# Kernel optimization log

Measured on AMD Instinct MI355X. Metric: run time of the kernel, lower is better.

The kernel has to match this reference:

```python
import jax, jax.numpy as jnp
import numpy as np

CHUNK = 64


def setup_inputs() -> dict:
    key = jax.random.key(0)
    ks = jax.random.split(key, 5)
    B, H, S, K, V = 2, 8, 8192, 128, 128
    q = jax.random.normal(ks[0], (B, H, S, K), jnp.float32)
    k = jax.random.normal(ks[1], (B, H, S, K), jnp.float32)
    v = jax.random.normal(ks[2], (B, H, S, V), jnp.float32)
    # decay gate is a (typically negative) log-decay
    g = -0.1 * jax.random.uniform(ks[3], (B, H, S), jnp.float32)
    beta = jax.random.uniform(ks[4], (B, H, S), jnp.float32)
    return {"q": q, "k": k, "v": v, "g": g, "beta": beta}


def _gated_delta_chunkwise(q, k, v, g, beta, chunk_size=CHUNK):
    B, H, S, K = q.shape
    V = v.shape[-1]
    scale = K ** -0.5
    # L2-normalize q/k, scale q
    q = q / (jnp.linalg.norm(q, axis=-1, keepdims=True) + 1e-6)
    k = k / (jnp.linalg.norm(k, axis=-1, keepdims=True) + 1e-6)
    q = (q * scale).astype(jnp.float32)
    k = k.astype(jnp.float32)
    v = v.astype(jnp.float32)
    g = g.astype(jnp.float32)
    beta = beta.astype(jnp.float32)

    BT = chunk_size
    assert S % BT == 0, "seq_len must be a multiple of chunk_size in this reference"
    N = S // BT
    # reshape into chunks: [N, B, H, BT, ...]
    qc = jnp.transpose(q.reshape(B, H, N, BT, K), (2, 0, 1, 3, 4))
    kc = jnp.transpose(k.reshape(B, H, N, BT, K), (2, 0, 1, 3, 4))
    vc = jnp.transpose(v.reshape(B, H, N, BT, V), (2, 0, 1, 3, 4))
    gc = jnp.transpose(g.reshape(B, H, N, BT), (2, 0, 1, 3))
    bc = jnp.transpose(beta.reshape(B, H, N, BT), (2, 0, 1, 3))

    gc = jnp.cumsum(gc, axis=-1)            # within-chunk cumulative log-decay
    eg = jnp.exp(gc)                        # [N,B,H,BT]

    # pairwise relative decay within chunk: d[i,j] = g_i - g_j  (<=0 for j<=i when g is non-increasing)
    d = gc[..., :, None] - gc[..., None, :]          # [N,B,H,BT,BT]
    de = jnp.minimum(d, 0.0)
    strict = jnp.tril(jnp.ones((BT, BT), bool), -1)
    incl = jnp.tril(jnp.ones((BT, BT), bool), 0)
    exp_s = jnp.exp(jnp.where(strict, de, -jnp.inf))  # strictly lower
    exp_i = jnp.exp(jnp.where(incl, de, -jnp.inf))    # inclusive lower

    # M = I + beta_i * (k_i . k_j) * exp(g_i - g_j), strictly lower triangular
    A0 = jnp.einsum('nbhik,nbhjk->nbhij', kc, kc) * exp_s * bc[..., :, None]
    M = jnp.eye(BT, dtype=jnp.float32) + A0
    Aqk = jnp.einsum('nbhik,nbhjk->nbhij', qc, kc) * exp_i

    # WY solve: M [w|u] = [beta*k*exp(g) | beta*v]
    rhs = jnp.concatenate([bc[..., None] * kc * eg[..., None], bc[..., None] * vc], axis=-1)
    solved = jax.lax.linalg.triangular_solve(M, rhs, left_side=True, lower=True, unit_diagonal=True)
    w = solved[..., :K]
    u = solved[..., K:]

    S0 = jnp.zeros((B, H, K, V), jnp.float32)

    def step(St, inp):
        q_i, k_i, u_i, g_i, w_i, A_i, eg_i = inp
        v_i = u_i - jnp.einsum('bhck,bhkv->bhcv', w_i, St)
        o_inter = jnp.einsum('bhck,bhkv->bhcv', q_i * eg_i[..., None], St)
        o_intra = jnp.einsum('bhij,bhjv->bhiv', A_i, v_i)
        o = o_inter + o_intra
        eg_last = eg_i[:, :, -1]
        ratio = jnp.where(eg_i > 0.0, eg_last[:, :, None] / eg_i, 0.0)
        S_new = St * eg_last[..., None, None] + jnp.einsum('bhck,bhcv->bhkv', ratio[..., None] * k_i, v_i)
        return S_new, o

    Sf, oc = jax.lax.scan(step, S0, (qc, kc, u, gc, w, Aqk, eg))
    o = jnp.transpose(oc, (1, 2, 0, 3, 4)).reshape(B, H, S, V)
    return o, Sf


def reference(q, k, v, g, beta):
    return _gated_delta_chunkwise(q, k, v, g, beta)
```

## Files before the change

### kernel.cpp

```cpp
#include <hip/hip_runtime.h>
#include <hip/hip_bf16.h>

typedef __bf16 bf16_t;
typedef bf16_t bf16x8 __attribute__((ext_vector_type(8)));
typedef float  f32x4  __attribute__((ext_vector_type(4)));

#define MFMA16(a, b, c) __builtin_amdgcn_mfma_f32_16x16x32_bf16((a), (b), (c), 0, 0, 0)

static constexpr int BH_N  = 16;
static constexpr int S_LEN = 8192;
static constexpr int KD    = 128;
static constexpr int VD    = 128;
static constexpr int BT    = 64;
static constexpr int NCH   = S_LEN / BT;
static constexpr int NT    = BH_N * NCH;

static constexpr size_t WS_W_OFF   = 0;
static constexpr size_t WS_Q_OFF   = WS_W_OFF   + (size_t)NT*BT*KD*2;
static constexpr size_t WS_KRT_OFF = WS_Q_OFF   + (size_t)NT*BT*KD*2;
static constexpr size_t WS_AQK_OFF = WS_KRT_OFF + (size_t)NT*KD*BT*2;
static constexpr size_t WS_U_OFF   = WS_AQK_OFF + (size_t)NT*BT*BT*2;
static constexpr size_t WS_EGL_OFF = WS_U_OFF   + (size_t)NT*BT*KD*4;

__global__ __launch_bounds__(256) void gdn_pre(
    const float* __restrict__ qg, const float* __restrict__ kg, const float* __restrict__ vg,
    const float* __restrict__ gg, const float* __restrict__ bg,
    bf16_t* __restrict__ wsW, bf16_t* __restrict__ wsQ, bf16_t* __restrict__ wsKrT,
    bf16_t* __restrict__ wsAqk, float* __restrict__ wsU, float* __restrict__ wsEgl)
{
    __shared__ bf16_t sKb[64][136];
    __shared__ bf16_t sQb[64][136];
    __shared__ float  sA0[64][64];
    __shared__ float  sGc[64];
    __shared__ float  sEg[64];
    __shared__ float  sBeta[64];

    const int tid  = threadIdx.x;
    const int lane = tid & 63;
    const int wid  = tid >> 6;
    const int tile = blockIdx.x;
    const int bh   = tile >> 7;
    const int c    = tile & 127;
    const size_t rowbase = (size_t)bh * S_LEN + (size_t)c * BT;

    if (wid == 0) {
        float val = gg[rowbase + lane];
        #pragma unroll
        for (int off = 1; off < 64; off <<= 1) {
            float t = __shfl_up(val, off);
            if (lane >= off) val += t;
        }
        sGc[lane] = val;
        sEg[lane] = expf(val);
    } else if (wid == 1) {
        sBeta[lane] = bg[rowbase + lane];
    }

    {
        const int r = tid >> 2;
        const int p = tid & 3;
        const float4* kp = reinterpret_cast<const float4*>(kg + (rowbase + r) * KD + p * 32);
        float4 kv[8];
        float ss = 0.f;
        #pragma unroll
        for (int ii = 0; ii < 8; ++ii) {
            kv[ii] = kp[ii];
            ss += kv[ii].x*kv[ii].x + kv[ii].y*kv[ii].y + kv[ii].z*kv[ii].z + kv[ii].w*kv[ii].w;
        }
        ss += __shfl_xor(ss, 1);
        ss += __shfl_xor(ss, 2);
        float inv = 1.f / (sqrtf(ss) + 1e-6f);
        #pragma unroll
        for (int ii = 0; ii < 8; ++ii) {
            int cb = p * 32 + ii * 4;
            sKb[r][cb+0] = (bf16_t)(kv[ii].x * inv);
            sKb[r][cb+1] = (bf16_t)(kv[ii].y * inv);
            sKb[r][cb+2] = (bf16_t)(kv[ii].z * inv);
            sKb[r][cb+3] = (bf16_t)(kv[ii].w * inv);
        }
        const float4* qp = reinterpret_cast<const float4*>(qg + (rowbase + r) * KD + p * 32);
        float4 qv[8];
        ss = 0.f;
        #pragma unroll
        for (int ii = 0; ii < 8; ++ii) {
            qv[ii] = qp[ii];
            ss += qv[ii].x*qv[ii].x + qv[ii].y*qv[ii].y + qv[ii].z*qv[ii].z + qv[ii].w*qv[ii].w;
        }
        ss += __shfl_xor(ss, 1);
        ss += __shfl_xor(ss, 2);
        inv = 0.08838834764831845f / (sqrtf(ss) + 1e-6f);
        #pragma unroll
        for (int ii = 0; ii < 8; ++ii) {
            int cb = p * 32 + ii * 4;
            sQb[r][cb+0] = (bf16_t)(qv[ii].x * inv);
            sQb[r][cb+1] = (bf16_t)(qv[ii].y * inv);
            sQb[r][cb+2] = (bf16_t)(qv[ii].z * inv);
            sQb[r][cb+3] = (bf16_t)(qv[ii].w * inv);
        }
    }
    __syncthreads();

    {
        const int frow = lane & 15;
        const int kgrp = (lane >> 4) * 8;
        f32x4 accK[4], accQ[4];
        #pragma unroll
        for (int n = 0; n < 4; ++n) { accK[n] = (f32x4){0.f,0.f,0.f,0.f}; accQ[n] = (f32x4){0.f,0.f,0.f,0.f}; }
        #pragma unroll
        for (int kk = 0; kk < 4; ++kk) {
            bf16x8 aK = *(const bf16x8*)&sKb[wid*16 + frow][kk*32 + kgrp];
            bf16x8 aQ = *(const bf16x8*)&sQb[wid*16 + frow][kk*32 + kgrp];
            #pragma unroll
            for (int n = 0; n < 4; ++n) {
                bf16x8 b = *(const bf16x8*)&sKb[n*16 + frow][kk*32 + kgrp];
                accK[n] = MFMA16(aK, b, accK[n]);
                accQ[n] = MFMA16(aQ, b, accQ[n]);
            }
        }
        const int crow = wid*16 + (lane >> 4) * 4;
        bf16_t* aqkBase = wsAqk + (size_t)tile * BT * BT;
        #pragma unroll
        for (int n = 0; n < 4; ++n) {
            #pragma unroll
            for (int r4 = 0; r4 < 4; ++r4) {
                int i = crow + r4, j = n*16 + frow;
                float e = expf(fminf(sGc[i] - sGc[j], 0.f));
                sA0[i][j] = (j < i) ? accK[n][r4] * e * sBeta[i] : 0.f;
                float aq  = (j <= i) ? accQ[n][r4] * e : 0.f;
                aqkBase[i * BT + j] = (bf16_t)aq;
            }
        }
    }

    {
        bf16_t* qb = wsQ   + (size_t)tile * BT * KD;
        bf16_t* kb = wsKrT + (size_t)tile * KD * BT;
        #pragma unroll
        for (int it = 0; it < 32; ++it) {
            int idx = tid + it * 256;
            int i = idx >> 7, m = idx & 127;
            qb[idx] = (bf16_t)((float)sQb[i][m] * sEg[i]);
        }
        #pragma unroll
        for (int it = 0; it < 32; ++it) {
            int idx = tid + it * 256;
            int m = idx >> 6, i = idx & 63;
            float ratio = expf(sGc[63] - sGc[i]);
            kb[idx] = (bf16_t)((float)sKb[i][m] * ratio);
        }
        if (tid == 0) wsEgl[tile] = sEg[63];
    }
    __syncthreads();

    {
        float x[64];
        if (tid < 128) {
            #pragma unroll
            for (int i = 0; i < 64; ++i)
                x[i] = sBeta[i] * sEg[i] * (float)sKb[i][tid];
        } else {
            const float* vp = vg + rowbase * VD + (tid - 128);
            #pragma unroll
            for (int i = 0; i < 64; ++i)
                x[i] = sBeta[i] * vp[(size_t)i * VD];
        }
        #pragma unroll
        for (int i = 1; i < 64; ++i) {
            float acc = x[i];
            #pragma unroll
            for (int j = 0; j < i; ++j)
                acc = fmaf(-sA0[i][j], x[j], acc);
            x[i] = acc;
        }
        if (tid < 128) {
            bf16_t* wp = wsW + (size_t)tile * BT * KD + tid;
            #pragma unroll
            for (int i = 0; i < 64; ++i) wp[(size_t)i * KD] = (bf16_t)x[i];
        } else {
            float* up = wsU + (size_t)tile * BT * KD + (tid - 128);
            #pragma unroll
            for (int i = 0; i < 64; ++i) up[(size_t)i * KD] = x[i];
        }
    }
}

__global__ __launch_bounds__(256) void gdn_scan(
    const bf16_t* __restrict__ wsW, const bf16_t* __restrict__ wsQ,
    const bf16_t* __restrict__ wsKrT, const bf16_t* __restrict__ wsAqk,
    const float* __restrict__ wsU, const float* __restrict__ wsEgl,
    float* __restrict__ outO, float* __restrict__ outS)
{
    __shared__ bf16_t sW[64][136];
    __shared__ bf16_t sQ[64][136];
    __shared__ bf16_t sKrT[128][72];
    __shared__ bf16_t sAqk[64][72];
    __shared__ bf16_t sSbT[32][136];
    __shared__ bf16_t sVbT[32][72];
    __shared__ float  sS[128][33];
    __shared__ float  sU[64][36];

    const int tid  = threadIdx.x;
    const int lane = tid & 63;
    const int wid  = tid >> 6;
    const int bh   = blockIdx.x >> 2;
    const int vb   = blockIdx.x & 3;
    const int col0 = vb * 32;
    const int frow = lane & 15;
    const int kgrp = (lane >> 4) * 8;

    {
        float* sSf = &sS[0][0];
        for (int it = tid; it < 128 * 33; it += 256) sSf[it] = 0.f;
    }
    __syncthreads();

    for (int c = 0; c < NCH; ++c) {
        const int tile = bh * NCH + c;
        {
            const ushort4* srcW = (const ushort4*)(wsW + (size_t)tile * BT * KD);
            const ushort4* srcQ = (const ushort4*)(wsQ + (size_t)tile * BT * KD);
            #pragma unroll
            for (int it = 0; it < 8; ++it) {
                int idx = tid + it * 256; int e0 = idx * 4; int rr = e0 >> 7; int m0 = e0 & 127;
                *(ushort4*)&sW[rr][m0] = srcW[idx];
                *(ushort4*)&sQ[rr][m0] = srcQ[idx];
            }
            const ushort4* srcKr = (const ushort4*)(wsKrT + (size_t)tile * KD * BT);
            #pragma unroll
            for (int it = 0; it < 8; ++it) {
                int idx = tid + it * 256; int e0 = idx * 4; int mm = e0 >> 6; int i0 = e0 & 63;
                *(ushort4*)&sKrT[mm][i0] = srcKr[idx];
            }
            const ushort4* srcAq = (const ushort4*)(wsAqk + (size_t)tile * BT * BT);
            #pragma unroll
            for (int it = 0; it < 4; ++it) {
                int idx = tid + it * 256; int e0 = idx * 4; int ii = e0 >> 6; int j0 = e0 & 63;
                *(ushort4*)&sAqk[ii][j0] = srcAq[idx];
            }
            const float* srcU = wsU + (size_t)tile * BT * KD;
            #pragma unroll
            for (int it = 0; it < 2; ++it) {
                int idx = tid + it * 256; int r = idx >> 3; int qq = idx & 7;
                *(float4*)&sU[r][qq * 4] = *(const float4*)(srcU + (size_t)r * KD + col0 + qq * 4);
            }
        }
        #pragma unroll
        for (int it = 0; it < 16; ++it) {
            int idx = tid + it * 256;
            int j = idx >> 7, m = idx & 127;
            sSbT[j][m] = (bf16_t)sS[m][j];
        }
        __syncthreads();

        f32x4 accW[2], accO[2];
        accW[0] = (f32x4){0.f,0.f,0.f,0.f}; accW[1] = accW[0];
        accO[0] = accW[0];                  accO[1] = accW[0];
        #pragma unroll
        for (int kk = 0; kk < 4; ++kk) {
            bf16x8 aW = *(const bf16x8*)&sW[wid*16 + frow][kk*32 + kgrp];
            bf16x8 aQ = *(const bf16x8*)&sQ[wid*16 + frow][kk*32 + kgrp];
            #pragma unroll
            for (int n = 0; n < 2; ++n) {
                bf16x8 b = *(const bf16x8*)&sSbT[n*16 + frow][kk*32 + kgrp];
                accW[n] = MFMA16(aW, b, accW[n]);
                accO[n] = MFMA16(aQ, b, accO[n]);
            }
        }
        {
            const int crow = wid*16 + (lane >> 4) * 4;
            #pragma unroll
            for (int n = 0; n < 2; ++n)
                #pragma unroll
                for (int r4 = 0; r4 < 4; ++r4) {
                    int i = crow + r4, j = n*16 + frow;
                    sVbT[j][i] = (bf16_t)(sU[i][j] - accW[n][r4]);
                }
        }
        __syncthreads();

        #pragma unroll
        for (int kk = 0; kk < 2; ++kk) {
            bf16x8 aA = *(const bf16x8*)&sAqk[wid*16 + frow][kk*32 + kgrp];
            #pragma unroll
            for (int n = 0; n < 2; ++n) {
                bf16x8 b = *(const bf16x8*)&sVbT[n*16 + frow][kk*32 + kgrp];
                accO[n] = MFMA16(aA, b, accO[n]);
            }
        }
        {
            const int crow = wid*16 + (lane >> 4) * 4;
            float* ob = outO + ((size_t)bh * S_LEN + (size_t)c * BT) * VD + col0;
            #pragma unroll
            for (int n = 0; n < 2; ++n)
                #pragma unroll
                for (int r4 = 0; r4 < 4; ++r4) {
                    int i = crow + r4, j = n*16 + frow;
                    ob[(size_t)i * VD + j] = accO[n][r4];
                }
        }
        {
            const float egl = wsEgl[tile];
            #pragma unroll
            for (int mt = 0; mt < 2; ++mt) {
                const int mrowA = wid*32 + mt*16 + frow;
                const int mrowC = wid*32 + mt*16 + (lane >> 4) * 4;
                f32x4 accS[2];
                #pragma unroll
                for (int n = 0; n < 2; ++n)
                    #pragma unroll
                    for (int r4 = 0; r4 < 4; ++r4)
                        accS[n][r4] = egl * sS[mrowC + r4][n*16 + frow];
                #pragma unroll
                for (int kk = 0; kk < 2; ++kk) {
                    bf16x8 aK = *(const bf16x8*)&sKrT[mrowA][kk*32 + kgrp];
                    #pragma unroll
                    for (int n = 0; n < 2; ++n) {
                        bf16x8 b = *(const bf16x8*)&sVbT[n*16 + frow][kk*32 + kgrp];
                        accS[n] = MFMA16(aK, b, accS[n]);
                    }
                }
                #pragma unroll
                for (int n = 0; n < 2; ++n)
                    #pragma unroll
                    for (int r4 = 0; r4 < 4; ++r4)
                        sS[mrowC + r4][n*16 + frow] = accS[n][r4];
            }
        }
        __syncthreads();
    }

    {
        float* sb = outS + (size_t)bh * KD * VD + col0;
        #pragma unroll
        for (int it = 0; it < 16; ++it) {
            int idx = tid + it * 256;
            int m = idx >> 5, j = idx & 31;
            sb[(size_t)m * VD + j] = sS[m][j];
        }
    }
}

extern "C" void kernel_launch(void* const* d_in, const int* in_sizes, int n_in,
                              void* d_out, int out_size, void* d_ws, size_t ws_size,
                              hipStream_t stream) {
    (void)in_sizes; (void)n_in; (void)out_size; (void)ws_size;
    const float* q    = (const float*)d_in[0];
    const float* k    = (const float*)d_in[1];
    const float* v    = (const float*)d_in[2];
    const float* g    = (const float*)d_in[3];
    const float* beta = (const float*)d_in[4];

    char* ws = (char*)d_ws;
    bf16_t* wsW   = (bf16_t*)(ws + WS_W_OFF);
    bf16_t* wsQ   = (bf16_t*)(ws + WS_Q_OFF);
    bf16_t* wsKrT = (bf16_t*)(ws + WS_KRT_OFF);
    bf16_t* wsAqk = (bf16_t*)(ws + WS_AQK_OFF);
    float*  wsU   = (float*)(ws + WS_U_OFF);
    float*  wsEgl = (float*)(ws + WS_EGL_OFF);

    float* outO = (float*)d_out;
    float* outS = outO + (size_t)BH_N * S_LEN * VD;

    gdn_pre<<<dim3(NT), dim3(256), 0, stream>>>(q, k, v, g, beta,
                                                wsW, wsQ, wsKrT, wsAqk, wsU, wsEgl);
    gdn_scan<<<dim3(BH_N * 4), dim3(256), 0, stream>>>(wsW, wsQ, wsKrT, wsAqk, wsU, wsEgl,
                                                       outO, outS);
}
```

Baseline: 624.4 us.

## Keep scan state in registers and prefetch next chunk fragments directly from global

The scan kernel no longer stages W, Q, KrT, Aqk and U through shared memory. Each lane loads its MFMA fragments straight from global into a register double buffer, prefetching chunk c+1 while chunk c is computed, and the running state S stays in registers with only a bf16 transposed copy written to shared memory. Block indices are remapped so the four V-column blocks of a head share an XCD. The pre kernel also precomputes the decay ratios once and vectorises the Q and K output writes. The intent is to cut LDS traffic and barriers on the serial critical path and to hide global load latency, at the cost of higher register pressure.

```diff
diff --git a/kernel.cpp b/kernel.cpp
--- a/kernel.cpp
+++ b/kernel.cpp
@@ -3,6 +3,7 @@
 
 typedef __bf16 bf16_t;
 typedef bf16_t bf16x8 __attribute__((ext_vector_type(8)));
+typedef bf16_t bf16x4 __attribute__((ext_vector_type(4)));
 typedef float  f32x4  __attribute__((ext_vector_type(4)));
 
 #define MFMA16(a, b, c) __builtin_amdgcn_mfma_f32_16x16x32_bf16((a), (b), (c), 0, 0, 0)
@@ -33,6 +34,7 @@
     __shared__ float  sA0[64][64];
     __shared__ float  sGc[64];
     __shared__ float  sEg[64];
+    __shared__ float  sRatio[64];
     __shared__ float  sBeta[64];
 
     const int tid  = threadIdx.x;
@@ -50,8 +52,11 @@
             float t = __shfl_up(val, off);
             if (lane >= off) val += t;
         }
-        sGc[lane] = val;
-        sEg[lane] = expf(val);
+        float g63 = __shfl(val, 63);
+        sGc[lane]    = val;
+        sEg[lane]    = expf(val);
+        sRatio[lane] = expf(g63 - val);
+        if (lane == 0) wsEgl[tile] = expf(g63);
     } else if (wid == 1) {
         sBeta[lane] = bg[rowbase + lane];
     }
@@ -136,19 +141,27 @@
         bf16_t* qb = wsQ   + (size_t)tile * BT * KD;
         bf16_t* kb = wsKrT + (size_t)tile * KD * BT;
         #pragma unroll
-        for (int it = 0; it < 32; ++it) {
-            int idx = tid + it * 256;
-            int i = idx >> 7, m = idx & 127;
-            qb[idx] = (bf16_t)((float)sQb[i][m] * sEg[i]);
-        }
-        #pragma unroll
-        for (int it = 0; it < 32; ++it) {
-            int idx = tid + it * 256;
-            int m = idx >> 6, i = idx & 63;
-            float ratio = expf(sGc[63] - sGc[i]);
-            kb[idx] = (bf16_t)((float)sKb[i][m] * ratio);
-        }
-        if (tid == 0) wsEgl[tile] = sEg[63];
+        for (int it = 0; it < 4; ++it) {
+            int e0 = (tid + it * 256) * 8;
+            int i = e0 >> 7, m0 = e0 & 127;
+            float eg = sEg[i];
+            bf16x8 src = *(const bf16x8*)&sQb[i][m0];
+            bf16x8 dst;
+            #pragma unroll
+            for (int jj = 0; jj < 8; ++jj) dst[jj] = (bf16_t)((float)src[jj] * eg);
+            *(bf16x8*)&qb[e0] = dst;
+        }
+        const int i  = tid & 63;
+        const int mg = tid >> 6;
+        float ratio = sRatio[i];
+        #pragma unroll
+        for (int it = 0; it < 4; ++it) {
+            int m0 = mg * 8 + it * 32;
+            bf16x8 s = *(const bf16x8*)&sKb[i][m0];
+            #pragma unroll
+            for (int jj = 0; jj < 8; ++jj)
+                kb[(m0 + jj) * BT + i] = (bf16_t)((float)s[jj] * ratio);
+        }
     }
     __syncthreads();
 
@@ -183,6 +196,15 @@
         }
     }
 }
+
+struct Frag {
+    bf16x8 w[4];
+    bf16x8 q[4];
+    bf16x8 kr[4];
+    bf16x8 aq[2];
+    float  u[8];
+    float  egl;
+};
 
 __global__ __launch_bounds__(256) void gdn_scan(
     const bf16_t* __restrict__ wsW, const bf16_t* __restrict__ wsQ,
@@ -190,154 +212,132 @@
     const float* __restrict__ wsU, const float* __restrict__ wsEgl,
     float* __restrict__ outO, float* __restrict__ outS)
 {
-    __shared__ bf16_t sW[64][136];
-    __shared__ bf16_t sQ[64][136];
-    __shared__ bf16_t sKrT[128][72];
-    __shared__ bf16_t sAqk[64][72];
     __shared__ bf16_t sSbT[32][136];
     __shared__ bf16_t sVbT[32][72];
-    __shared__ float  sS[128][33];
-    __shared__ float  sU[64][36];
 
     const int tid  = threadIdx.x;
     const int lane = tid & 63;
     const int wid  = tid >> 6;
-    const int bh   = blockIdx.x >> 2;
-    const int vb   = blockIdx.x & 3;
+    const int idx = blockIdx.x;
+    const int xcd = idx & 7;
+    const int vb  = (idx >> 3) & 3;
+    const int bh  = xcd + ((idx >> 5) << 3);
     const int col0 = vb * 32;
     const int frow = lane & 15;
-    const int kgrp = (lane >> 4) * 8;
-
-    {
-        float* sSf = &sS[0][0];
-        for (int it = tid; it < 128 * 33; it += 256) sSf[it] = 0.f;
-    }
-    __syncthreads();
-
-    for (int c = 0; c < NCH; ++c) {
-        const int tile = bh * NCH + c;
-        {
-            const ushort4* srcW = (const ushort4*)(wsW + (size_t)tile * BT * KD);
-            const ushort4* srcQ = (const ushort4*)(wsQ + (size_t)tile * BT * KD);
-            #pragma unroll
-            for (int it = 0; it < 8; ++it) {
-                int idx = tid + it * 256; int e0 = idx * 4; int rr = e0 >> 7; int m0 = e0 & 127;
-                *(ushort4*)&sW[rr][m0] = srcW[idx];
-                *(ushort4*)&sQ[rr][m0] = srcQ[idx];
-            }
-            const ushort4* srcKr = (const ushort4*)(wsKrT + (size_t)tile * KD * BT);
-            #pragma unroll
-            for (int it = 0; it < 8; ++it) {
-                int idx = tid + it * 256; int e0 = idx * 4; int mm = e0 >> 6; int i0 = e0 & 63;
-                *(ushort4*)&sKrT[mm][i0] = srcKr[idx];
-            }
-            const ushort4* srcAq = (const ushort4*)(wsAqk + (size_t)tile * BT * BT);
-            #pragma unroll
-            for (int it = 0; it < 4; ++it) {
-                int idx = tid + it * 256; int e0 = idx * 4; int ii = e0 >> 6; int j0 = e0 & 63;
-                *(ushort4*)&sAqk[ii][j0] = srcAq[idx];
-            }
-            const float* srcU = wsU + (size_t)tile * BT * KD;
-            #pragma unroll
-            for (int it = 0; it < 2; ++it) {
-                int idx = tid + it * 256; int r = idx >> 3; int qq = idx & 7;
-                *(float4*)&sU[r][qq * 4] = *(const float4*)(srcU + (size_t)r * KD + col0 + qq * 4);
-            }
-        }
-        #pragma unroll
-        for (int it = 0; it < 16; ++it) {
-            int idx = tid + it * 256;
-            int j = idx >> 7, m = idx & 127;
-            sSbT[j][m] = (bf16_t)sS[m][j];
-        }
-        __syncthreads();
-
-        f32x4 accW[2], accO[2];
-        accW[0] = (f32x4){0.f,0.f,0.f,0.f}; accW[1] = accW[0];
-        accO[0] = accW[0];                  accO[1] = accW[0];
-        #pragma unroll
-        for (int kk = 0; kk < 4; ++kk) {
-            bf16x8 aW = *(const bf16x8*)&sW[wid*16 + frow][kk*32 + kgrp];
-            bf16x8 aQ = *(const bf16x8*)&sQ[wid*16 + frow][kk*32 + kgrp];
-            #pragma unroll
-            for (int n = 0; n < 2; ++n) {
-                bf16x8 b = *(const bf16x8*)&sSbT[n*16 + frow][kk*32 + kgrp];
-                accW[n] = MFMA16(aW, b, accW[n]);
-                accO[n] = MFMA16(aQ, b, accO[n]);
-            }
-        }
-        {
-            const int crow = wid*16 + (lane >> 4) * 4;
+    const int hi   = lane >> 4;
+    const int kgrp = hi * 8;
+    const int rowWQ = wid * 16 + frow;
+    const int crow  = wid * 16 + hi * 4;
+    const int mrowA = wid * 32 + frow;
+    const int mrowC = wid * 32 + hi * 4;
+
+    f32x4 Sreg[2][2];
+    #pragma unroll
+    for (int mt = 0; mt < 2; ++mt)
+        #pragma unroll
+        for (int n = 0; n < 2; ++n) Sreg[mt][n] = (f32x4){0.f,0.f,0.f,0.f};
+
+    {
+        uint* z = (uint*)&sSbT[0][0];
+        for (int i = tid; i < 32*136/2; i += 256) z[i] = 0u;
+    }
+
+#define PREFETCH(F, TILE) do {                                                   \
+    const size_t _t = (TILE);                                                    \
+    const bf16_t* pW = wsW + _t*BT*KD + rowWQ*KD + kgrp;                         \
+    const bf16_t* pQ = wsQ + _t*BT*KD + rowWQ*KD + kgrp;                         \
+    _Pragma("unroll") for (int kk = 0; kk < 4; ++kk) {                           \
+        (F).w[kk] = *(const bf16x8*)(pW + kk*32);                                \
+        (F).q[kk] = *(const bf16x8*)(pQ + kk*32);                                \
+    }                                                                            \
+    const bf16_t* pA = wsAqk + _t*BT*BT + rowWQ*BT + kgrp;                       \
+    _Pragma("unroll") for (int kk = 0; kk < 2; ++kk)                             \
+        (F).aq[kk] = *(const bf16x8*)(pA + kk*32);                               \
+    const bf16_t* pK = wsKrT + _t*KD*BT + mrowA*BT + kgrp;                       \
+    _Pragma("unroll") for (int mt = 0; mt < 2; ++mt)                             \
+        _Pragma("unroll") for (int kk = 0; kk < 2; ++kk)                         \
+            (F).kr[mt*2+kk] = *(const bf16x8*)(pK + mt*16*BT + kk*32);           \
+    const float* pU = wsU + _t*BT*KD + (size_t)crow*KD + col0 + frow;            \
+    _Pragma("unroll") for (int n = 0; n < 2; ++n)                                \
+        _Pragma("unroll") for (int r4 = 0; r4 < 4; ++r4)                         \
+            (F).u[n*4+r4] = pU[r4*KD + n*16];                                    \
+    (F).egl = wsEgl[_t];                                                         \
+} while (0)
+
+#define STEP(CUR, NXT, C) do {                                                   \
+    int _cn = (C) + 1; if (_cn > NCH-1) _cn = NCH-1;                             \
+    PREFETCH(NXT, (size_t)bh*NCH + _cn);                                         \
+    __syncthreads();                            \
+    f32x4 accW[2], accO[2];                                                      \
+    accW[0] = (f32x4){0.f,0.f,0.f,0.f}; accW[1] = accW[0];                       \
+    accO[0] = accW[0];                  accO[1] = accW[0];                       \
+    _Pragma("unroll") for (int kk = 0; kk < 4; ++kk) {                           \
+        _Pragma("unroll") for (int n = 0; n < 2; ++n) {                          \
+            bf16x8 bS = *(const bf16x8*)&sSbT[n*16 + frow][kk*32 + kgrp];        \
+            accW[n] = MFMA16((CUR).w[kk], bS, accW[n]);                          \
+            accO[n] = MFMA16((CUR).q[kk], bS, accO[n]);                          \
+        }                                                                        \
+    }                                                                            \
+    _Pragma("unroll") for (int n = 0; n < 2; ++n) {                              \
+        bf16x4 pk;                                                               \
+        _Pragma("unroll") for (int r4 = 0; r4 < 4; ++r4)                         \
+            pk[r4] = (bf16_t)((CUR).u[n*4+r4] - accW[n][r4]);                    \
+        *(bf16x4*)&sVbT[n*16 + frow][crow] = pk;                                 \
+    }                                                                            \
+    __syncthreads();                                             \
+    _Pragma("unroll") for (int kk = 0; kk < 2; ++kk) {                           \
+        _Pragma("unroll") for (int n = 0; n < 2; ++n) {                          \
+            bf16x8 bV = *(const bf16x8*)&sVbT[n*16 + frow][kk*32 + kgrp];        \
+            accO[n] = MFMA16((CUR).aq[kk], bV, accO[n]);                         \
+        }                                                                        \
+    }                                                                            \
+    {                                                                            \
+        float* ob = outO + ((size_t)bh*S_LEN + (size_t)(C)*BT)*VD + col0;        \
+        _Pragma("unroll") for (int n = 0; n < 2; ++n)                            \
+            _Pragma("unroll") for (int r4 = 0; r4 < 4; ++r4)                     \
+                ob[(size_t)(crow + r4)*VD + n*16 + frow] = accO[n][r4];          \
+    }                                                                            \
+    _Pragma("unroll") for (int mt = 0; mt < 2; ++mt) {                           \
+        f32x4 accS[2];                                                           \
+        _Pragma("unroll") for (int n = 0; n < 2; ++n)                            \
+            _Pragma("unroll") for (int r4 = 0; r4 < 4; ++r4)                     \
+                accS[n][r4] = (CUR).egl * Sreg[mt][n][r4];                       \
+        _Pragma("unroll") for (int kk = 0; kk < 2; ++kk) {                       \
+            _Pragma("unroll") for (int n = 0; n < 2; ++n) {                      \
+                bf16x8 bV = *(const bf16x8*)&sVbT[n*16 + frow][kk*32 + kgrp];    \
+                accS[n] = MFMA16((CUR).kr[mt*2+kk], bV, accS[n]);                \
+            }                                                                    \
+        }                                                                        \
+        _Pragma("unroll") for (int n = 0; n < 2; ++n) {                          \
+            bf16x4 pk;                                                           \
+            _Pragma("unroll") for (int r4 = 0; r4 < 4; ++r4)                     \
+                pk[r4] = (bf16_t)accS[n][r4];                                    \
+            *(bf16x4*)&sSbT[n*16 + frow][mrowC + mt*16] = pk;                    \
+            Sreg[mt][n] = accS[n];                                               \
+        }                                                                        \
+    }                                                                            \
+} while (0)
+
+    Frag fA, fB;
+    PREFETCH(fA, (size_t)bh*NCH + 0);
+
+    for (int c = 0; c < NCH; c += 2) {
+        STEP(fA, fB, c);
+        STEP(fB, fA, c + 1);
+    }
+
+    {
+        float* sb = outS + (size_t)bh * KD * VD + col0;
+        #pragma unroll
+        for (int mt = 0; mt < 2; ++mt)
             #pragma unroll
             for (int n = 0; n < 2; ++n)
                 #pragma unroll
-                for (int r4 = 0; r4 < 4; ++r4) {
-                    int i = crow + r4, j = n*16 + frow;
-                    sVbT[j][i] = (bf16_t)(sU[i][j] - accW[n][r4]);
-                }
-        }
-        __syncthreads();
-
-        #pragma unroll
-        for (int kk = 0; kk < 2; ++kk) {
-            bf16x8 aA = *(const bf16x8*)&sAqk[wid*16 + frow][kk*32 + kgrp];
-            #pragma unroll
-            for (int n = 0; n < 2; ++n) {
-                bf16x8 b = *(const bf16x8*)&sVbT[n*16 + frow][kk*32 + kgrp];
-                accO[n] = MFMA16(aA, b, accO[n]);
-            }
-        }
-        {
-            const int crow = wid*16 + (lane >> 4) * 4;
-            float* ob = outO + ((size_t)bh * S_LEN + (size_t)c * BT) * VD + col0;
-            #pragma unroll
-            for (int n = 0; n < 2; ++n)
-                #pragma unroll
-                for (int r4 = 0; r4 < 4; ++r4) {
-                    int i = crow + r4, j = n*16 + frow;
-                    ob[(size_t)i * VD + j] = accO[n][r4];
-                }
-        }
-        {
-            const float egl = wsEgl[tile];
-            #pragma unroll
-            for (int mt = 0; mt < 2; ++mt) {
-                const int mrowA = wid*32 + mt*16 + frow;
-                const int mrowC = wid*32 + mt*16 + (lane >> 4) * 4;
-                f32x4 accS[2];
-                #pragma unroll
-                for (int n = 0; n < 2; ++n)
-                    #pragma unroll
-                    for (int r4 = 0; r4 < 4; ++r4)
-                        accS[n][r4] = egl * sS[mrowC + r4][n*16 + frow];
-                #pragma unroll
-                for (int kk = 0; kk < 2; ++kk) {
-                    bf16x8 aK = *(const bf16x8*)&sKrT[mrowA][kk*32 + kgrp];
-                    #pragma unroll
-                    for (int n = 0; n < 2; ++n) {
-                        bf16x8 b = *(const bf16x8*)&sVbT[n*16 + frow][kk*32 + kgrp];
-                        accS[n] = MFMA16(aK, b, accS[n]);
-                    }
-                }
-                #pragma unroll
-                for (int n = 0; n < 2; ++n)
-                    #pragma unroll
-                    for (int r4 = 0; r4 < 4; ++r4)
-                        sS[mrowC + r4][n*16 + frow] = accS[n][r4];
-            }
-        }
-        __syncthreads();
-    }
-
-    {
-        float* sb = outS + (size_t)bh * KD * VD + col0;
-        #pragma unroll
-        for (int it = 0; it < 16; ++it) {
-            int idx = tid + it * 256;
-            int m = idx >> 5, j = idx & 31;
-            sb[(size_t)m * VD + j] = sS[m][j];
-        }
-    }
+                for (int r4 = 0; r4 < 4; ++r4)
+                    sb[(size_t)(mrowC + mt*16 + r4) * VD + n*16 + frow] = Sreg[mt][n][r4];
+    }
+#undef STEP
+#undef PREFETCH
 }
 
 extern "C" void kernel_launch(void* const* d_in, const int* in_sizes, int n_in,
```

New measurement: 504.4 us. 19.2% less time.
